# Performance work log

Measured on AMD Instinct MI355X. Metric: run time of the kernel, lower is better.

Reference implementation:

```python
import jax, jax.numpy as jnp
import numpy as np
from jax import lax

B, S, D, H = 8, 1024, 512, 8
K = 25  # moving-average kernel
EPS = 1e-6


def setup_inputs() -> dict:
    key = jax.random.key(0)
    ks = jax.random.split(key, 8)

    def dense_w(k, din, dout):
        return (jax.random.normal(k, (din, dout), jnp.float32) / np.sqrt(din).astype(np.float32))

    return {
        "x": jax.random.normal(ks[0], (B, S, D), jnp.float32),
        "wq": dense_w(ks[1], D, D), "bq": jnp.zeros((D,), jnp.float32),
        "wk": dense_w(ks[2], D, D), "bk": jnp.zeros((D,), jnp.float32),
        "wv": dense_w(ks[3], D, D), "bv": jnp.zeros((D,), jnp.float32),
        "wo": dense_w(ks[4], D, D), "bo": jnp.zeros((D,), jnp.float32),
        "w1": dense_w(ks[5], D, 4 * D), "b1": jnp.zeros((4 * D,), jnp.float32),
        "w2": dense_w(ks[6], 4 * D, D), "b2": jnp.zeros((D,), jnp.float32),
        "g1": jnp.ones((D,), jnp.float32), "be1": jnp.zeros((D,), jnp.float32),
        "g2": jnp.ones((D,), jnp.float32), "be2": jnp.zeros((D,), jnp.float32),
        "g3": jnp.ones((D,), jnp.float32), "be3": jnp.zeros((D,), jnp.float32),
        "num_heads": H,
    }


def _moving_avg(x):
    # TF AveragePooling1D(pool=K, stride=1, padding='same'): divisor excludes padding.
    s = lax.reduce_window(x, 0.0, lax.add, (1, K, 1), (1, 1, 1), 'SAME')
    cnt = lax.reduce_window(jnp.ones((1, x.shape[1], 1), x.dtype), 0.0, lax.add,
                            (1, K, 1), (1, 1, 1), 'SAME')
    return s / cnt


def _layernorm(x, g, b):
    m = jnp.mean(x, -1, keepdims=True)
    v = jnp.var(x, -1, keepdims=True)
    return (x - m) * jax.lax.rsqrt(v + EPS) * g + b


def _auto_correlation(x, wq, bq, wk, bk, wv, bv, wo, bo, num_heads):
    b, s, d = x.shape
    dp = d // num_heads
    def split_heads(t):
        return t.reshape(b, s, num_heads, dp).transpose(0, 2, 1, 3)  # [B,H,S,dp]
    q = split_heads(x @ wq + bq)
    k = split_heads(x @ wk + bk)
    v = split_heads(x @ wv + bv)
    # Faithful to source: rfft over innermost (depth) axis, fft_length = 2*S.
    qf = jnp.fft.rfft(q, n=2 * s, axis=-1)
    kf = jnp.fft.rfft(k, n=2 * s, axis=-1)
    corr = jnp.fft.irfft(qf * jnp.conj(kf), n=2 * s, axis=-1)[..., :s]  # [B,H,S,S]
    scale = 1.0 / np.sqrt(dp).astype(np.float32)
    attn = jax.nn.softmax(scale * corr, axis=-1)
    out = jnp.einsum('bhst,bhtd->bhsd', attn, v)
    out = out.transpose(0, 2, 1, 3).reshape(b, s, d)
    return out @ wo + bo


def reference(x, wq, bq, wk, bk, wv, bv, wo, bo, w1, b1, w2, b2,
              g1, be1, g2, be2, g3, be3, num_heads):
    trend_init = _moving_avg(x)
    seasonal_init = x - trend_init
    attn_out = _auto_correlation(seasonal_init, wq, bq, wk, bk, wv, bv, wo, bo, num_heads)
    out1 = _layernorm(attn_out + seasonal_init, g1, be1)
    ffn = jax.nn.relu(out1 @ w1 + b1) @ w2 + b2
    seasonal_out = _layernorm(out1 + ffn, g2, be2) + seasonal_init
    trend2 = _moving_avg(seasonal_out)
    seasonal_final = seasonal_out - trend2
    x_out = seasonal_final + (trend2 + trend_init)
    return _layernorm(x_out, g3, be3)
```

## Files before the change

kernel.cpp:

```cpp
#include <hip/hip_runtime.h>
#include <cstdint>


typedef float f32x4 __attribute__((ext_vector_type(4)));
typedef __bf16 bf16x8 __attribute__((ext_vector_type(8)));
typedef _Float16 h2t __attribute__((ext_vector_type(2)));
typedef unsigned short u16;
typedef unsigned int u32;
typedef u32 u32x4 __attribute__((ext_vector_type(4)));

__device__ __forceinline__ u16 f2bf(float f) {
  unsigned int u = __float_as_uint(f);
  u = (u + 0x7FFFu + ((u >> 16) & 1u)) >> 16;
  return (u16)u;
}

__device__ __forceinline__ float bf2f(u16 b) { return __uint_as_float((u32)b << 16); }

__device__ __forceinline__ u16 f2h(float f) {
  _Float16 hv = (_Float16)f;
  u16 b;
  __builtin_memcpy(&b, &hv, 2);
  return b;
}

__device__ __forceinline__ float dot2h(u32 qp, u32 kp_, float c) {
#if __has_builtin(__builtin_amdgcn_fdot2)
  return __builtin_amdgcn_fdot2(__builtin_bit_cast(h2t, qp),
                                __builtin_bit_cast(h2t, kp_), c, false);
#else
  h2t q = __builtin_bit_cast(h2t, qp), k = __builtin_bit_cast(h2t, kp_);
  c = fmaf((float)q.x, (float)k.x, c);
  return fmaf((float)q.y, (float)k.y, c);
#endif
}

__device__ __forceinline__ void gload_lds16(const void* g, void* l) {
  __builtin_amdgcn_global_load_lds((__attribute__((address_space(1))) void*)g,
                                   (__attribute__((address_space(3))) void*)l,
                                   16, 0, 0);
}

__global__ __launch_bounds__(256) void movavg_kernel(
    const float* __restrict__ x, u16* __restrict__ seas_bf,
    u16* __restrict__ a64, float* __restrict__ srow) {
  int blk = blockIdx.x;
  int sc = blk & 127, b = blk >> 7;
  int d = threadIdx.x * 2;
  const float* xb = x + (size_t)b * 1024 * 512 + d;
  int s0 = sc * 8;
  int lo = max(s0 - 12, 0), hi = min(s0 + 12, 1023);
  float sx = 0.f, sy = 0.f;
  for (int j = lo; j <= hi; ++j) {
    float2 v = *(const float2*)&xb[(size_t)j * 512];
    sx += v.x;
    sy += v.y;
  }
  float ax = 0.f, ay = 0.f;
#pragma unroll
  for (int s = s0; s < s0 + 8; ++s) {
    int l2 = max(s - 12, 0), h2 = min(s + 12, 1023);
    float invc = 1.f / (float)(h2 - l2 + 1);
    float2 xv = *(const float2*)&xb[(size_t)s * 512];
    float sex = xv.x - sx * invc;
    float sey = xv.y - sy * invc;
    size_t idx = (size_t)(b * 1024 + s) * 512 + d;
    u32 pk = (u32)f2bf(sex) | ((u32)f2bf(sey) << 16);
    *(u32*)&seas_bf[idx] = pk;
    if (s < 64) *(u32*)&a64[(size_t)(b * 64 + s) * 512 + d] = pk;
    ax += sex;
    ay += sey;
    if (s - 12 >= 0) {
      float2 v = *(const float2*)&xb[(size_t)(s - 12) * 512];
      sx -= v.x;
      sy -= v.y;
    }
    if (s + 13 <= 1023) {
      float2 v = *(const float2*)&xb[(size_t)(s + 13) * 512];
      sx += v.x;
      sy += v.y;
    }
  }
  atomicAdd(&srow[b * 512 + d], ax);
  atomicAdd(&srow[b * 512 + d + 1], ay);
}

__global__ __launch_bounds__(256) void weights_prep_kernel(
    const float* __restrict__ wq, const float* __restrict__ wk,
    const float* __restrict__ wv, const float* __restrict__ wo,
    const float* __restrict__ w1, const float* __restrict__ w2,
    const float* __restrict__ bq, const float* __restrict__ bk,
    u16* __restrict__ wqkt, u16* __restrict__ wvt, u16* __restrict__ wot,
    u16* __restrict__ w1t, u16* __restrict__ w2t, float* __restrict__ qkbias) {
  __shared__ float tile[32][33];
  int i = blockIdx.x;
  int tx = threadIdx.x, ty = threadIdx.y;
  if (i >= 3072) {
    int idx = (i - 3072) * 256 + ty * 32 + tx;
    qkbias[idx] = idx < 512 ? bq[idx] : bk[idx - 512];
    return;
  }
  const float* src;
  u16* dst;
  int R, C, bx, by;
  if (i < 1024) {
    int w = i >> 8, l = i & 255;
    src = (w == 0 ? wq : w == 1 ? wk : w == 2 ? wv : wo);
    dst = (w == 0 ? wqkt : w == 1 ? wqkt + 512 * 512 : w == 2 ? wvt : wot);
    R = 512; C = 512; bx = l & 15; by = l >> 4;
  } else if (i < 2048) {
    int l = i - 1024;
    src = w1; dst = w1t; R = 512; C = 2048; bx = l & 15; by = l >> 4;
  } else {
    int l = i - 2048;
    src = w2; dst = w2t; R = 2048; C = 512; bx = l & 63; by = l >> 6;
  }
  int r0 = bx * 32, c0 = by * 32;
#pragma unroll
  for (int k = 0; k < 4; ++k)
    tile[ty + 8 * k][tx] = src[(size_t)(r0 + ty + 8 * k) * C + c0 + tx];
  __syncthreads();
#pragma unroll
  for (int k = 0; k < 4; ++k)
    dst[(size_t)(c0 + ty + 8 * k) * R + r0 + tx] = f2bf(tile[tx][ty + 8 * k]);
}

__global__ __launch_bounds__(256) void vsum_kernel(
    const float* __restrict__ srow, const float* __restrict__ wv,
    const float* __restrict__ bv, float* __restrict__ vsum) {
  int blk = blockIdx.x;
  int b = blk >> 1;
  int n = (blk & 1) * 256 + threadIdx.x;
  float acc = 0.f;
  for (int k = 0; k < 512; ++k) acc += srow[b * 512 + k] * wv[(size_t)k * 512 + n];
  vsum[b * 512 + n] = acc + 1024.f * bv[n];
}

template <int RELU, int OMODE, int KSPLIT>
__global__ __launch_bounds__(512, 1) void gemm8p_kernel(
    const u16* __restrict__ A, const u16* __restrict__ Bt,
    const float* __restrict__ bias, void* __restrict__ Cv, void* __restrict__ Cv2,
    int M, int N, int K) {
  __shared__ u16 As[3][2][256 * 32];
  __shared__ u16 Bs[3][2][128 * 32];
  const int tid = threadIdx.x;
  const int wid = tid >> 6, lane = tid & 63;
  const int wm = wid >> 2, wn = wid & 3;
  const int la = lane & 15, lg = lane >> 4;
  int nwg = gridDim.x * gridDim.y;
  int lin = blockIdx.y * gridDim.x + blockIdx.x;
  int swz = (lin & 7) * (nwg >> 3) + (lin >> 3);
  int bx = swz / gridDim.y, by = swz % gridDim.y;
  const int row0 = bx * 256, col0 = by * 128;
  const int z = (KSPLIT > 1) ? (int)blockIdx.z : 0;
  const int kbeg = z * (K / KSPLIT);
  const int nt = (K / KSPLIT) / 64;
  f32x4 acc[8][2] = {};

  auto stageh = [&](int buf, int h, int k0) {
    int kh = k0 + h * 32;
    {
      int p = tid, r = p >> 2, cg = (p & 3) ^ ((r >> 1) & 3);
      gload_lds16(A + (size_t)(row0 + r) * K + kh + cg * 8,
                  ((char*)&As[buf][h][0]) + p * 16);
    }
    {
      int p = tid + 512, r = p >> 2, cg = (p & 3) ^ ((r >> 1) & 3);
      gload_lds16(A + (size_t)(row0 + r) * K + kh + cg * 8,
                  ((char*)&As[buf][h][0]) + p * 16);
    }
    {
      int p = tid, r = p >> 2, cg = (p & 3) ^ ((r >> 1) & 3);
      gload_lds16(Bt + (size_t)(col0 + r) * K + kh + cg * 8,
                  ((char*)&Bs[buf][h][0]) + p * 16);
    }
  };

  stageh(0, 0, kbeg);
  stageh(0, 1, kbeg);
  stageh(1, 0, kbeg + 64);
  stageh(1, 1, kbeg + 64);
  asm volatile("s_waitcnt vmcnt(6)" ::: "memory");
  __builtin_amdgcn_s_barrier();
  __builtin_amdgcn_sched_barrier(0);

  for (int t = 0; t < nt; ++t) {
    const int buf = t % 3;
    const int nbuf = (t + 2) % 3;
    const bool pre = (t + 2 < nt);
#pragma unroll
    for (int h = 0; h < 2; ++h) {
      bf16x8 af[8], bf[2];
#pragma unroll
      for (int mf = 0; mf < 8; ++mf) {
        int r = wm * 128 + mf * 16 + la;
        int cp = lg ^ ((r >> 1) & 3);
        af[mf] = *(const bf16x8*)&As[buf][h][r * 32 + cp * 8];
      }
#pragma unroll
      for (int nf = 0; nf < 2; ++nf) {
        int r = wn * 32 + nf * 16 + la;
        int cp = lg ^ ((r >> 1) & 3);
        bf[nf] = *(const bf16x8*)&Bs[buf][h][r * 32 + cp * 8];
      }
      if (pre) stageh(nbuf, h, kbeg + (t + 2) * 64);
      __builtin_amdgcn_sched_barrier(0);
      __builtin_amdgcn_s_barrier();
      __builtin_amdgcn_s_setprio(1);
#pragma unroll
      for (int mf = 0; mf < 8; ++mf)
#pragma unroll
        for (int nf = 0; nf < 2; ++nf)
          acc[mf][nf] = __builtin_amdgcn_mfma_f32_16x16x32_bf16(af[mf], bf[nf], acc[mf][nf], 0, 0, 0);
      __builtin_amdgcn_s_setprio(0);
      __builtin_amdgcn_sched_barrier(0);
      if (h == 0) __builtin_amdgcn_s_barrier();
    }
    if (pre)
      asm volatile("s_waitcnt vmcnt(6)" ::: "memory");
    else if (t + 1 < nt)
      asm volatile("s_waitcnt vmcnt(0)" ::: "memory");
    __builtin_amdgcn_s_barrier();
    __builtin_amdgcn_sched_barrier(0);
  }

  void* Cout = (z == 0) ? Cv : Cv2;
#pragma unroll
  for (int mf = 0; mf < 8; ++mf) {
    int r = row0 + wm * 128 + mf * 16 + lg * 4;
#pragma unroll
    for (int nf = 0; nf < 2; ++nf) {
      int cc = col0 + wn * 32 + nf * 16 + la;
      float bvv = (z == 0) ? bias[cc] : 0.f;
#pragma unroll
      for (int j = 0; j < 4; ++j) {
        float v = acc[mf][nf][j] + bvv;
        if (RELU) v = fmaxf(v, 0.f);
        if constexpr (OMODE == 1)
          ((u16*)Cout)[(size_t)(r + j) * N + cc] = f2bf(v);
        else
          ((u16*)Cout)[(size_t)(r + j) * N + cc] = f2h(v);
      }
    }
  }
}

__global__ __launch_bounds__(256, 6) void gemm_v_kernel(
    const u16* __restrict__ A, const u16* __restrict__ Bt,
    const float* __restrict__ bias, u16* __restrict__ Cv, int M, int N, int K) {
  constexpr int BK = 32;
  __shared__ u16 As[2][128 * BK];
  __shared__ u16 Bs[2][64 * BK];
  const int tid = threadIdx.x;
  const int wid = tid >> 6, lane = tid & 63;
  const int wm = wid >> 1, wn = wid & 1;
  const int la = lane & 15, lg = lane >> 4;
  const int row0 = blockIdx.x * 128, col0 = blockIdx.y * 64;
  const int ksteps = K / BK;
  f32x4 acc[4][2] = {};

  auto stage = [&](int buf, int k0) {
    {
      int p = tid, r = p >> 2, cg = (p & 3) ^ ((r >> 1) & 3);
      gload_lds16(A + (size_t)(row0 + r) * K + k0 + cg * 8, ((char*)As[buf]) + p * 16);
    }
    {
      int p = tid + 256, r = p >> 2, cg = (p & 3) ^ ((r >> 1) & 3);
      gload_lds16(A + (size_t)(row0 + r) * K + k0 + cg * 8, ((char*)As[buf]) + p * 16);
    }
    {
      int p = tid, r = p >> 2, cg = (p & 3) ^ ((r >> 1) & 3);
      gload_lds16(Bt + (size_t)(col0 + r) * K + k0 + cg * 8, ((char*)Bs[buf]) + p * 16);
    }
  };

  stage(0, 0);
  __syncthreads();
  for (int t = 0; t < ksteps; ++t) {
    const int cur = t & 1;
    if (t + 1 < ksteps) stage(cur ^ 1, (t + 1) * BK);
    bf16x8 af[4], bfr[2];
#pragma unroll
    for (int m = 0; m < 4; ++m) {
      int r = wm * 64 + m * 16 + la;
      int cp = lg ^ ((r >> 1) & 3);
      af[m] = *(const bf16x8*)(((const char*)As[cur]) + r * 64 + cp * 16);
    }
#pragma unroll
    for (int n = 0; n < 2; ++n) {
      int r = wn * 32 + n * 16 + la;
      int cp = lg ^ ((r >> 1) & 3);
      bfr[n] = *(const bf16x8*)(((const char*)Bs[cur]) + r * 64 + cp * 16);
    }
#pragma unroll
    for (int m = 0; m < 4; ++m)
#pragma unroll
      for (int n = 0; n < 2; ++n)
        acc[m][n] = __builtin_amdgcn_mfma_f32_16x16x32_bf16(af[m], bfr[n], acc[m][n], 0, 0, 0);
    __syncthreads();
  }

#pragma unroll
  for (int m = 0; m < 4; ++m) {
    int r = row0 + wm * 64 + m * 16 + lg * 4;
#pragma unroll
    for (int n = 0; n < 2; ++n) {
      int cc = col0 + wn * 32 + n * 16 + la;
      float bvv = bias[cc];
#pragma unroll
      for (int j = 0; j < 4; ++j) {
        float v = acc[m][n][j] + bvv;
        int rr = r + j;
        int bb = rr >> 6, tt = rr & 63, hh = cc >> 6, dd = cc & 63;
        Cv[(((size_t)bb * 8 + hh) * 64 + dd) * 64 + tt] = f2bf(v);
      }
    }
  }
}

__global__ __launch_bounds__(256) void attn_mfma_kernel(
    const u16* __restrict__ qk, const u16* __restrict__ v64t,
    const float* __restrict__ vsum, u16* __restrict__ attn_bf) {
  __shared__ u32 qE[32][64];
  __shared__ u32 qO[32][64];
  __shared__ u32 kp[32][32];
  __shared__ u16 coef[32][64];
  __shared__ u16 vtt[64][64];
  __shared__ float zc[32];
  __shared__ float Vs[64];
  int bid = blockIdx.x;
  int scnk = bid & 31, h = (bid >> 5) & 7, b = bid >> 8;
  int tid = threadIdx.x, wid = tid >> 6, lane = tid & 63;
  int bh = b * 8 + h;

  {
    int p = tid, r = p >> 3, cc = p & 7;
    gload_lds16(v64t + ((size_t)bh * 4096 + r * 64 + ((cc ^ (r & 7)) * 8)),
                ((char*)vtt) + p * 16);
    p = tid + 256; r = p >> 3; cc = p & 7;
    gload_lds16(v64t + ((size_t)bh * 4096 + r * 64 + ((cc ^ (r & 7)) * 8)),
                ((char*)vtt) + p * 16);
  }
  *(f32x4*)&qE[tid >> 3][32 + ((tid & 7) << 2)] = f32x4{};
  {
    int s = tid >> 3, c = tid & 7;
    size_t grow = ((size_t)(b * 1024 + scnk * 32 + s)) * 1024 + h * 64;
    *(f32x4*)&qE[s][c * 4] = *(const f32x4*)&qk[grow + c * 8];
    *(f32x4*)&kp[s][c * 4] = *(const f32x4*)&qk[grow + 512 + c * 8];
  }
  if (tid < 64) Vs[tid] = vsum[b * 512 + h * 64 + tid];
  __syncthreads();
  for (int j2 = tid; j2 < 1024; j2 += 256) {
    int s = j2 >> 5, j = j2 & 31;
    u32 a = qE[s][j], b2 = qE[s][j + 1];
    qO[s][j] = (a >> 16) | (b2 << 16);
    qO[s][j + 32] = 0;
  }
  __syncthreads();
  for (int i = 0; i < 8; ++i) {
    int s = wid * 8 + i;
    u32x4 kk4[8];
#pragma unroll
    for (int u = 0; u < 8; ++u) kk4[u] = *(const u32x4*)&kp[s][u * 4];
    int t = lane, sel = t & 1;
    const u32* qptr = (sel ? qO[s] : qE[s]) + (t >> 1);
    float c = 0.f;
#pragma unroll
    for (int u = 0; u < 8; ++u) {
#pragma unroll
      for (int v = 0; v < 4; ++v) c = dot2h(qptr[u * 4 + v], kk4[u][v], c);
    }
    float sc = c * 0.125f;
    float mx = fmaxf(sc, 0.f);
#pragma unroll
    for (int off = 32; off >= 1; off >>= 1) mx = fmaxf(mx, __shfl_xor(mx, off));
    float w = __expf(sc - mx), wz = __expf(-mx);
    float sw = w;
#pragma unroll
    for (int off = 32; off >= 1; off >>= 1) sw += __shfl_xor(sw, off);
    float inv = 1.f / (sw + 960.f * wz);
    *(u16*)(((char*)&coef[s][0]) + ((2 * t) ^ ((s & 7) << 4))) = f2bf((w - wz) * inv);
    if (lane == 0) zc[s] = wz * inv;
  }
  __syncthreads();
  {
    int sm = wid >> 1, nh = wid & 1;
    int la = lane & 15, lg = lane >> 4;
    int r = sm * 16 + la;
    int n0 = nh * 32 + la, n1 = nh * 32 + 16 + la;
    f32x4 acc0 = {}, acc1 = {};
#pragma unroll
    for (int ks = 0; ks < 2; ++ks) {
      int lr = ks * 4 + lg;
      bf16x8 af = *(const bf16x8*)(((const char*)coef) + r * 128 + ((lr ^ (r & 7)) << 4));
      bf16x8 bf0 = *(const bf16x8*)(((const char*)vtt) + n0 * 128 + ((lr ^ (n0 & 7)) << 4));
      bf16x8 bf1 = *(const bf16x8*)(((const char*)vtt) + n1 * 128 + ((lr ^ (n1 & 7)) << 4));
      acc0 = __builtin_amdgcn_mfma_f32_16x16x32_bf16(af, bf0, acc0, 0, 0, 0);
      acc1 = __builtin_amdgcn_mfma_f32_16x16x32_bf16(af, bf1, acc1, 0, 0, 0);
    }
    int srl0 = sm * 16 + lg * 4;
    int srow0 = b * 1024 + scnk * 32 + srl0;
    float vs0 = Vs[nh * 32 + la], vs1 = Vs[nh * 32 + 16 + la];
#pragma unroll
    for (int j = 0; j < 4; ++j) {
      float zcv = zc[srl0 + j];
      size_t rb = (size_t)(srow0 + j) * 512 + h * 64;
      attn_bf[rb + nh * 32 + la] = f2bf(acc0[j] + zcv * vs0);
      attn_bf[rb + nh * 32 + 16 + la] = f2bf(acc1[j] + zcv * vs1);
    }
  }
}

__device__ __forceinline__ void block_reduce_2(float& a, float& b, float* sbuf) {
  int tid = threadIdx.x, wid = tid >> 6, lane = tid & 63;
#pragma unroll
  for (int off = 32; off >= 1; off >>= 1) {
    a += __shfl_xor(a, off);
    b += __shfl_xor(b, off);
  }
  if (lane == 0) {
    sbuf[wid] = a;
    sbuf[4 + wid] = b;
  }
  __syncthreads();
  a = sbuf[0] + sbuf[1] + sbuf[2] + sbuf[3];
  b = sbuf[4] + sbuf[5] + sbuf[6] + sbuf[7];
  __syncthreads();
}

__global__ __launch_bounds__(256) void ln_res_kernel(
    const u16* __restrict__ xa, const u16* __restrict__ xb,
    u16* __restrict__ res_out,
    const float* __restrict__ g, const float* __restrict__ be) {
  __shared__ float sbuf[8];
  int row = blockIdx.x, tid = threadIdx.x;
  int d = tid * 2;
  size_t base = (size_t)row * 512 + d;
  u32 pa = *(const u32*)&xa[base];
  u32 pb = *(const u32*)&xb[base];
  u32 pr = *(const u32*)&res_out[base];
  float v0 = bf2f((u16)pa) + bf2f((u16)pb) + bf2f((u16)pr);
  float v1 = bf2f((u16)(pa >> 16)) + bf2f((u16)(pb >> 16)) + bf2f((u16)(pr >> 16));
  float s = v0 + v1, q = v0 * v0 + v1 * v1;
  block_reduce_2(s, q, sbuf);
  float mean = s * (1.f / 512.f);
  float var = q * (1.f / 512.f) - mean * mean;
  float rs = rsqrtf(var + 1e-6f);
  float2 gg = *(const float2*)&g[d];
  float2 bb = *(const float2*)&be[d];
  float o0 = (v0 - mean) * rs * gg.x + bb.x;
  float o1 = (v1 - mean) * rs * gg.y + bb.y;
  *(u32*)&res_out[base] = (u32)f2bf(o0) | ((u32)f2bf(o1) << 16);
}

__global__ __launch_bounds__(256) void final_kernel(
    const u16* __restrict__ out1, const u16* __restrict__ fa,
    const u16* __restrict__ fb, const float* __restrict__ x,
    const float* __restrict__ g2, const float* __restrict__ be2,
    const float* __restrict__ g3, const float* __restrict__ be3,
    float* __restrict__ out) {
  __shared__ float sbuf[8];
  int row = blockIdx.x, tid = threadIdx.x;
  int d = tid * 2;
  size_t base = (size_t)row * 512 + d;
  u32 po = *(const u32*)&out1[base];
  u32 pa = *(const u32*)&fa[base];
  u32 pb = *(const u32*)&fb[base];
  float t0 = bf2f((u16)po) + bf2f((u16)pa) + bf2f((u16)pb);
  float t1 = bf2f((u16)(po >> 16)) + bf2f((u16)(pa >> 16)) + bf2f((u16)(pb >> 16));
  float s = t0 + t1, q = t0 * t0 + t1 * t1;
  block_reduce_2(s, q, sbuf);
  float mean = s * (1.f / 512.f);
  float var = q * (1.f / 512.f) - mean * mean;
  float rs = rsqrtf(var + 1e-6f);
  float2 g2v = *(const float2*)&g2[d];
  float2 b2v = *(const float2*)&be2[d];
  float2 xv = *(const float2*)&x[base];
  float y0 = (t0 - mean) * rs * g2v.x + b2v.x + xv.x;
  float y1 = (t1 - mean) * rs * g2v.y + b2v.y + xv.y;
  s = y0 + y1;
  q = y0 * y0 + y1 * y1;
  block_reduce_2(s, q, sbuf);
  mean = s * (1.f / 512.f);
  var = q * (1.f / 512.f) - mean * mean;
  rs = rsqrtf(var + 1e-6f);
  float2 g3v = *(const float2*)&g3[d];
  float2 b3v = *(const float2*)&be3[d];
  float2 o = make_float2((y0 - mean) * rs * g3v.x + b3v.x,
                         (y1 - mean) * rs * g3v.y + b3v.y);
  *(float2*)&out[base] = o;
}

extern "C" void kernel_launch(void* const* d_in, const int* in_sizes, int n_in,
                              void* d_out, int out_size, void* d_ws, size_t ws_size,
                              hipStream_t stream) {
  const float* x = (const float*)d_in[0];
  const float* wq = (const float*)d_in[1];
  const float* bq = (const float*)d_in[2];
  const float* wk = (const float*)d_in[3];
  const float* bk = (const float*)d_in[4];
  const float* wv = (const float*)d_in[5];
  const float* bv = (const float*)d_in[6];
  const float* wo = (const float*)d_in[7];
  const float* bo = (const float*)d_in[8];
  const float* w1 = (const float*)d_in[9];
  const float* b1 = (const float*)d_in[10];
  const float* w2 = (const float*)d_in[11];
  const float* b2 = (const float*)d_in[12];
  const float* g1 = (const float*)d_in[13];
  const float* be1 = (const float*)d_in[14];
  const float* g2 = (const float*)d_in[15];
  const float* be2 = (const float*)d_in[16];
  const float* g3 = (const float*)d_in[17];
  const float* be3 = (const float*)d_in[18];
  float* out = (float*)d_out;

  const size_t MS = 8192ull * 512ull;
  float* srow = (float*)d_ws;
  float* vsumb = srow + 4096;
  float* qkbias = vsumb + 4096;
  u16* qk_f16 = (u16*)(qkbias + 1024);
  u16* hidden = qk_f16 + 8192ull * 1024;
  u16* seas_bf = hidden + 8192ull * 2048;
  u16* attn_bf = seas_bf + MS;
  u16* wo0 = attn_bf + MS;
  u16* wo1 = wo0 + MS;
  u16* v64t = wo1 + MS;
  u16* a64_bf = v64t + 512 * 512;
  u16* wqkt = a64_bf + 512 * 512;
  u16* wvt = wqkt + 1024 * 512;
  u16* wot = wvt + 512 * 512;
  u16* w1t = wot + 512 * 512;
  u16* w2t = w1t + 2048ull * 512;
  u16* ff0 = qk_f16;
  u16* ff1 = ff0 + MS;

  hipMemsetAsync(srow, 0, 4096 * sizeof(float), stream);
  weights_prep_kernel<<<3076, dim3(32, 8), 0, stream>>>(
      wq, wk, wv, wo, w1, w2, bq, bk, wqkt, wvt, wot, w1t, w2t, qkbias);

  movavg_kernel<<<1024, 256, 0, stream>>>(x, seas_bf, a64_bf, srow);
  vsum_kernel<<<16, 256, 0, stream>>>(srow, wv, bv, vsumb);

  gemm8p_kernel<0, 2, 1><<<dim3(32, 8), 512, 0, stream>>>(
      seas_bf, wqkt, qkbias, qk_f16, nullptr, 8192, 1024, 512);
  gemm_v_kernel<<<dim3(4, 8), 256, 0, stream>>>(a64_bf, wvt, bv, v64t, 512, 512, 512);

  attn_mfma_kernel<<<2048, 256, 0, stream>>>(qk_f16, v64t, vsumb, attn_bf);

  gemm8p_kernel<0, 1, 2><<<dim3(32, 4, 2), 512, 0, stream>>>(
      attn_bf, wot, bo, wo0, wo1, 8192, 512, 512);
  ln_res_kernel<<<8192, 256, 0, stream>>>(wo0, wo1, seas_bf, g1, be1);

  gemm8p_kernel<1, 1, 1><<<dim3(32, 16), 512, 0, stream>>>(
      seas_bf, w1t, b1, hidden, nullptr, 8192, 2048, 512);
  gemm8p_kernel<0, 1, 2><<<dim3(32, 4, 2), 512, 0, stream>>>(
      hidden, w2t, b2, ff0, ff1, 8192, 512, 2048);

  final_kernel<<<8192, 256, 0, stream>>>(seas_bf, ff0, ff1, x, g2, be2, g3, be3, out);
}
```

Before: 212.3 us.

## Fuse QK projection GEMM with auto-correlation attention in one kernel

Replaces the separate Q/K projection GEMM and the attention kernel with one kernel. Each block computes the Q and K columns for one head over 256 rows, keeps the fp16 results in LDS, then runs the correlation, softmax and V product from that LDS tile. This removes the global round trip of the 8192x1024 qk_f16 intermediate and one kernel launch. In exchange it uses about 156KB of LDS, so only one block runs per CU, and the grid is just 256 blocks. The attention phase also runs serially over eight chunks inside each block.

```diff
diff --git a/kernel.cpp b/kernel.cpp
--- a/kernel.cpp
+++ b/kernel.cpp
@@ -236,12 +236,203 @@
       for (int j = 0; j < 4; ++j) {
         float v = acc[mf][nf][j] + bvv;
         if (RELU) v = fmaxf(v, 0.f);
-        if constexpr (OMODE == 1)
-          ((u16*)Cout)[(size_t)(r + j) * N + cc] = f2bf(v);
-        else
-          ((u16*)Cout)[(size_t)(r + j) * N + cc] = f2h(v);
-      }
-    }
+        ((u16*)Cout)[(size_t)(r + j) * N + cc] = f2bf(v);
+      }
+    }
+  }
+}
+
+__global__ __launch_bounds__(512, 1) void qkattn_kernel(
+    const u16* __restrict__ A, const u16* __restrict__ Wqk,
+    const float* __restrict__ qkb, const u16* __restrict__ v64t,
+    const float* __restrict__ vsum, u16* __restrict__ attn_bf) {
+  __shared__ __align__(16) char pool[156160];
+  u16* vtt = (u16*)(pool + 147456);
+  float* Vs = (float*)(pool + 155648);
+  float* zc = (float*)(pool + 155904);
+  u16* tile = (u16*)pool;
+  u32* qE = (u32*)(pool + 65536);
+  u32* qO = (u32*)(pool + 73728);
+  u32* kp = (u32*)(pool + 81920);
+  u16* coef = (u16*)(pool + 86016);
+
+  const int tid = threadIdx.x;
+  const int wid = tid >> 6, lane = tid & 63;
+  const int wm = wid >> 2, wn = wid & 3;
+  const int la = lane & 15, lg = lane >> 4;
+  const int K = 512;
+  int nwg = gridDim.x * gridDim.y;
+  int lin = blockIdx.y * gridDim.x + blockIdx.x;
+  int swz = (lin & 7) * (nwg >> 3) + (lin >> 3);
+  int bx = swz / gridDim.y, h = swz % gridDim.y;
+  const int row0 = bx * 256;
+  const int b = row0 >> 10;
+  const int bh = b * 8 + h;
+  f32x4 acc[8][2] = {};
+
+  {
+    int p = tid, r = p >> 3, cc = p & 7;
+    gload_lds16(v64t + ((size_t)bh * 4096 + r * 64 + ((cc ^ (r & 7)) * 8)),
+                ((char*)vtt) + p * 16);
+  }
+
+  auto stageh = [&](int buf, int hh, int k0) {
+    int kh = k0 + hh * 32;
+    char* abase = pool + (buf * 2 + hh) * 16384;
+    char* bbase = pool + 98304 + (buf * 2 + hh) * 8192;
+    {
+      int p = tid, r = p >> 2, cg = (p & 3) ^ ((r >> 1) & 3);
+      gload_lds16(A + (size_t)(row0 + r) * K + kh + cg * 8, abase + p * 16);
+    }
+    {
+      int p = tid + 512, r = p >> 2, cg = (p & 3) ^ ((r >> 1) & 3);
+      gload_lds16(A + (size_t)(row0 + r) * K + kh + cg * 8, abase + p * 16);
+    }
+    {
+      int p = tid, r = p >> 2, cg = (p & 3) ^ ((r >> 1) & 3);
+      int gr = (r < 64) ? h * 64 + r : 448 + h * 64 + r;
+      gload_lds16(Wqk + (size_t)gr * K + kh + cg * 8, bbase + p * 16);
+    }
+  };
+
+  stageh(0, 0, 0);
+  stageh(0, 1, 0);
+  stageh(1, 0, 64);
+  stageh(1, 1, 64);
+  asm volatile("s_waitcnt vmcnt(6)" ::: "memory");
+  __builtin_amdgcn_s_barrier();
+  __builtin_amdgcn_sched_barrier(0);
+
+  const int nt = 8;
+  for (int t = 0; t < nt; ++t) {
+    const int buf = t % 3, nbuf = (t + 2) % 3;
+    const bool pre = (t + 2 < nt);
+#pragma unroll
+    for (int hh = 0; hh < 2; ++hh) {
+      const char* ab = pool + (buf * 2 + hh) * 16384;
+      const char* bb = pool + 98304 + (buf * 2 + hh) * 8192;
+      bf16x8 af[8], bfv[2];
+#pragma unroll
+      for (int mf = 0; mf < 8; ++mf) {
+        int r = wm * 128 + mf * 16 + la;
+        int cp = lg ^ ((r >> 1) & 3);
+        af[mf] = *(const bf16x8*)(ab + r * 64 + cp * 16);
+      }
+#pragma unroll
+      for (int nf = 0; nf < 2; ++nf) {
+        int r = wn * 32 + nf * 16 + la;
+        int cp = lg ^ ((r >> 1) & 3);
+        bfv[nf] = *(const bf16x8*)(bb + r * 64 + cp * 16);
+      }
+      if (pre) stageh(nbuf, hh, (t + 2) * 64);
+      __builtin_amdgcn_sched_barrier(0);
+      __builtin_amdgcn_s_barrier();
+      __builtin_amdgcn_s_setprio(1);
+#pragma unroll
+      for (int mf = 0; mf < 8; ++mf)
+#pragma unroll
+        for (int nf = 0; nf < 2; ++nf)
+          acc[mf][nf] = __builtin_amdgcn_mfma_f32_16x16x32_bf16(af[mf], bfv[nf], acc[mf][nf], 0, 0, 0);
+      __builtin_amdgcn_s_setprio(0);
+      __builtin_amdgcn_sched_barrier(0);
+      if (hh == 0) __builtin_amdgcn_s_barrier();
+    }
+    if (pre)
+      asm volatile("s_waitcnt vmcnt(6)" ::: "memory");
+    else if (t + 1 < nt)
+      asm volatile("s_waitcnt vmcnt(0)" ::: "memory");
+    __builtin_amdgcn_s_barrier();
+    __builtin_amdgcn_sched_barrier(0);
+  }
+  if (tid < 64) Vs[tid] = vsum[b * 512 + h * 64 + tid];
+#pragma unroll
+  for (int mf = 0; mf < 8; ++mf) {
+    int r = wm * 128 + mf * 16 + lg * 4;
+#pragma unroll
+    for (int nf = 0; nf < 2; ++nf) {
+      int cc = wn * 32 + nf * 16 + la;
+      float bvv = qkb[(cc < 64) ? h * 64 + cc : 448 + h * 64 + cc];
+#pragma unroll
+      for (int j = 0; j < 4; ++j) {
+        int rr = r + j;
+        u32 byte = ((u32)(rr * 128 + cc) * 2) ^ ((u32)(rr & 7) << 4);
+        *(u16*)(((char*)tile) + byte) = f2h(acc[mf][nf][j] + bvv);
+      }
+    }
+  }
+  __builtin_amdgcn_s_barrier();
+
+  for (int c = 0; c < 8; ++c) {
+    int cr0 = c * 32;
+    for (int idx = tid; idx < 2048; idx += 512) {
+      int s = idx >> 6, j = idx & 63;
+      u32 v = 0;
+      if (j < 32) {
+        int rr = cr0 + s;
+        u32 byte = ((u32)(rr * 128 + 2 * j) * 2) ^ ((u32)(rr & 7) << 4);
+        v = *(const u32*)(((const char*)tile) + byte);
+      }
+      qE[s * 64 + j] = v;
+    }
+    for (int idx = tid; idx < 1024; idx += 512) {
+      int s = idx >> 5, m = idx & 31;
+      int rr = cr0 + s;
+      u32 byte = ((u32)(rr * 128 + 64 + 2 * m) * 2) ^ ((u32)(rr & 7) << 4);
+      kp[s * 32 + m] = *(const u32*)(((const char*)tile) + byte);
+    }
+    __builtin_amdgcn_s_barrier();
+    for (int idx = tid; idx < 1024; idx += 512) {
+      int s = idx >> 5, j = idx & 31;
+      u32 a = qE[s * 64 + j], b2 = qE[s * 64 + j + 1];
+      qO[s * 64 + j] = (a >> 16) | (b2 << 16);
+      qO[s * 64 + j + 32] = 0;
+    }
+    __builtin_amdgcn_s_barrier();
+    for (int i = 0; i < 4; ++i) {
+      int s = wid * 4 + i;
+      u32x4 kk4[8];
+#pragma unroll
+      for (int u = 0; u < 8; ++u) kk4[u] = *(const u32x4*)&kp[s * 32 + u * 4];
+      int t2 = lane, sel = t2 & 1;
+      const u32* qptr = (sel ? qO : qE) + s * 64 + (t2 >> 1);
+      float cv = 0.f;
+#pragma unroll
+      for (int u = 0; u < 8; ++u)
+#pragma unroll
+        for (int v = 0; v < 4; ++v) cv = dot2h(qptr[u * 4 + v], kk4[u][v], cv);
+      float sc = cv * 0.125f;
+      float mx = fmaxf(sc, 0.f);
+#pragma unroll
+      for (int off = 32; off >= 1; off >>= 1) mx = fmaxf(mx, __shfl_xor(mx, off));
+      float w = __expf(sc - mx), wz = __expf(-mx);
+      float sw = w;
+#pragma unroll
+      for (int off = 32; off >= 1; off >>= 1) sw += __shfl_xor(sw, off);
+      float inv = 1.f / (sw + 960.f * wz);
+      *(u16*)(((char*)coef) + ((s * 128 + 2 * t2) ^ ((s & 7) << 4))) = f2bf((w - wz) * inv);
+      if (lane == 0) zc[s] = wz * inv;
+    }
+    __builtin_amdgcn_s_barrier();
+    {
+      int sm = wid >> 2, nh = wid & 3;
+      int r = sm * 16 + la;
+      int n0 = nh * 16 + la;
+      f32x4 a0 = {};
+#pragma unroll
+      for (int ks = 0; ks < 2; ++ks) {
+        int lr = ks * 4 + lg;
+        bf16x8 af = *(const bf16x8*)(((const char*)coef) + r * 128 + ((lr ^ (r & 7)) << 4));
+        bf16x8 b0 = *(const bf16x8*)(((const char*)vtt) + n0 * 128 + ((lr ^ (n0 & 7)) << 4));
+        a0 = __builtin_amdgcn_mfma_f32_16x16x32_bf16(af, b0, a0, 0, 0, 0);
+      }
+      int srl0 = sm * 16 + lg * 4;
+      int srow0 = row0 + cr0 + srl0;
+      float vs0 = Vs[n0];
+#pragma unroll
+      for (int j = 0; j < 4; ++j)
+        attn_bf[(size_t)(srow0 + j) * 512 + h * 64 + n0] = f2bf(a0[j] + zc[srl0 + j] * vs0);
+    }
+    __builtin_amdgcn_s_barrier();
   }
 }
 
@@ -314,99 +505,6 @@
         int bb = rr >> 6, tt = rr & 63, hh = cc >> 6, dd = cc & 63;
         Cv[(((size_t)bb * 8 + hh) * 64 + dd) * 64 + tt] = f2bf(v);
       }
-    }
-  }
-}
-
-__global__ __launch_bounds__(256) void attn_mfma_kernel(
-    const u16* __restrict__ qk, const u16* __restrict__ v64t,
-    const float* __restrict__ vsum, u16* __restrict__ attn_bf) {
-  __shared__ u32 qE[32][64];
-  __shared__ u32 qO[32][64];
-  __shared__ u32 kp[32][32];
-  __shared__ u16 coef[32][64];
-  __shared__ u16 vtt[64][64];
-  __shared__ float zc[32];
-  __shared__ float Vs[64];
-  int bid = blockIdx.x;
-  int scnk = bid & 31, h = (bid >> 5) & 7, b = bid >> 8;
-  int tid = threadIdx.x, wid = tid >> 6, lane = tid & 63;
-  int bh = b * 8 + h;
-
-  {
-    int p = tid, r = p >> 3, cc = p & 7;
-    gload_lds16(v64t + ((size_t)bh * 4096 + r * 64 + ((cc ^ (r & 7)) * 8)),
-                ((char*)vtt) + p * 16);
-    p = tid + 256; r = p >> 3; cc = p & 7;
-    gload_lds16(v64t + ((size_t)bh * 4096 + r * 64 + ((cc ^ (r & 7)) * 8)),
-                ((char*)vtt) + p * 16);
-  }
-  *(f32x4*)&qE[tid >> 3][32 + ((tid & 7) << 2)] = f32x4{};
-  {
-    int s = tid >> 3, c = tid & 7;
-    size_t grow = ((size_t)(b * 1024 + scnk * 32 + s)) * 1024 + h * 64;
-    *(f32x4*)&qE[s][c * 4] = *(const f32x4*)&qk[grow + c * 8];
-    *(f32x4*)&kp[s][c * 4] = *(const f32x4*)&qk[grow + 512 + c * 8];
-  }
-  if (tid < 64) Vs[tid] = vsum[b * 512 + h * 64 + tid];
-  __syncthreads();
-  for (int j2 = tid; j2 < 1024; j2 += 256) {
-    int s = j2 >> 5, j = j2 & 31;
-    u32 a = qE[s][j], b2 = qE[s][j + 1];
-    qO[s][j] = (a >> 16) | (b2 << 16);
-    qO[s][j + 32] = 0;
-  }
-  __syncthreads();
-  for (int i = 0; i < 8; ++i) {
-    int s = wid * 8 + i;
-    u32x4 kk4[8];
-#pragma unroll
-    for (int u = 0; u < 8; ++u) kk4[u] = *(const u32x4*)&kp[s][u * 4];
-    int t = lane, sel = t & 1;
-    const u32* qptr = (sel ? qO[s] : qE[s]) + (t >> 1);
-    float c = 0.f;
-#pragma unroll
-    for (int u = 0; u < 8; ++u) {
-#pragma unroll
-      for (int v = 0; v < 4; ++v) c = dot2h(qptr[u * 4 + v], kk4[u][v], c);
-    }
-    float sc = c * 0.125f;
-    float mx = fmaxf(sc, 0.f);
-#pragma unroll
-    for (int off = 32; off >= 1; off >>= 1) mx = fmaxf(mx, __shfl_xor(mx, off));
-    float w = __expf(sc - mx), wz = __expf(-mx);
-    float sw = w;
-#pragma unroll
-    for (int off = 32; off >= 1; off >>= 1) sw += __shfl_xor(sw, off);
-    float inv = 1.f / (sw + 960.f * wz);
-    *(u16*)(((char*)&coef[s][0]) + ((2 * t) ^ ((s & 7) << 4))) = f2bf((w - wz) * inv);
-    if (lane == 0) zc[s] = wz * inv;
-  }
-  __syncthreads();
-  {
-    int sm = wid >> 1, nh = wid & 1;
-    int la = lane & 15, lg = lane >> 4;
-    int r = sm * 16 + la;
-    int n0 = nh * 32 + la, n1 = nh * 32 + 16 + la;
-    f32x4 acc0 = {}, acc1 = {};
-#pragma unroll
-    for (int ks = 0; ks < 2; ++ks) {
-      int lr = ks * 4 + lg;
-      bf16x8 af = *(const bf16x8*)(((const char*)coef) + r * 128 + ((lr ^ (r & 7)) << 4));
-      bf16x8 bf0 = *(const bf16x8*)(((const char*)vtt) + n0 * 128 + ((lr ^ (n0 & 7)) << 4));
-      bf16x8 bf1 = *(const bf16x8*)(((const char*)vtt) + n1 * 128 + ((lr ^ (n1 & 7)) << 4));
-      acc0 = __builtin_amdgcn_mfma_f32_16x16x32_bf16(af, bf0, acc0, 0, 0, 0);
-      acc1 = __builtin_amdgcn_mfma_f32_16x16x32_bf16(af, bf1, acc1, 0, 0, 0);
-    }
-    int srl0 = sm * 16 + lg * 4;
-    int srow0 = b * 1024 + scnk * 32 + srl0;
-    float vs0 = Vs[nh * 32 + la], vs1 = Vs[nh * 32 + 16 + la];
-#pragma unroll
-    for (int j = 0; j < 4; ++j) {
-      float zcv = zc[srl0 + j];
-      size_t rb = (size_t)(srow0 + j) * 512 + h * 64;
-      attn_bf[rb + nh * 32 + la] = f2bf(acc0[j] + zcv * vs0);
-      attn_bf[rb + nh * 32 + 16 + la] = f2bf(acc1[j] + zcv * vs1);
     }
   }
 }
@@ -519,8 +617,8 @@
   float* srow = (float*)d_ws;
   float* vsumb = srow + 4096;
   float* qkbias = vsumb + 4096;
-  u16* qk_f16 = (u16*)(qkbias + 1024);
-  u16* hidden = qk_f16 + 8192ull * 1024;
+  u16* ffbuf = (u16*)(qkbias + 1024);
+  u16* hidden = ffbuf + 2 * MS;
   u16* seas_bf = hidden + 8192ull * 2048;
   u16* attn_bf = seas_bf + MS;
   u16* wo0 = attn_bf + MS;
@@ -532,7 +630,7 @@
   u16* wot = wvt + 512 * 512;
   u16* w1t = wot + 512 * 512;
   u16* w2t = w1t + 2048ull * 512;
-  u16* ff0 = qk_f16;
+  u16* ff0 = ffbuf;
   u16* ff1 = ff0 + MS;
 
   hipMemsetAsync(srow, 0, 4096 * sizeof(float), stream);
@@ -542,11 +640,9 @@
   movavg_kernel<<<1024, 256, 0, stream>>>(x, seas_bf, a64_bf, srow);
   vsum_kernel<<<16, 256, 0, stream>>>(srow, wv, bv, vsumb);
 
-  gemm8p_kernel<0, 2, 1><<<dim3(32, 8), 512, 0, stream>>>(
-      seas_bf, wqkt, qkbias, qk_f16, nullptr, 8192, 1024, 512);
   gemm_v_kernel<<<dim3(4, 8), 256, 0, stream>>>(a64_bf, wvt, bv, v64t, 512, 512, 512);
-
-  attn_mfma_kernel<<<2048, 256, 0, stream>>>(qk_f16, v64t, vsumb, attn_bf);
+  qkattn_kernel<<<dim3(32, 8), 512, 0, stream>>>(
+      seas_bf, wqkt, qkbias, v64t, vsumb, attn_bf);
 
   gemm8p_kernel<0, 1, 2><<<dim3(32, 4, 2), 512, 0, stream>>>(
       attn_bf, wot, bo, wo0, wo1, 8192, 512, 512);
```

New measurement: 212.5 us. No clear change (+0.1%).

## Merge moving-average into prep kernel, halve attention row chunk, unroll vsum

Applied to the files above, without the earlier changes.

Folds the moving-average/seasonal kernel into the weight-prep launch as extra blocks, which removes one kernel launch and lets the two independent jobs run concurrently. The attention kernel now handles 16 query rows per block instead of 32 and launches twice as many blocks, for more parallelism and less shared memory per block, at the cost of reloading the V tile more often. The vsum reduction is split across eight independent FMA accumulators to expose more instruction-level parallelism.

```diff
diff --git a/kernel.cpp b/kernel.cpp
--- a/kernel.cpp
+++ b/kernel.cpp
@@ -41,62 +41,63 @@
                                    16, 0, 0);
 }
 
-__global__ __launch_bounds__(256) void movavg_kernel(
-    const float* __restrict__ x, u16* __restrict__ seas_bf,
-    u16* __restrict__ a64, float* __restrict__ srow) {
-  int blk = blockIdx.x;
-  int sc = blk & 127, b = blk >> 7;
-  int d = threadIdx.x * 2;
-  const float* xb = x + (size_t)b * 1024 * 512 + d;
-  int s0 = sc * 8;
-  int lo = max(s0 - 12, 0), hi = min(s0 + 12, 1023);
-  float sx = 0.f, sy = 0.f;
-  for (int j = lo; j <= hi; ++j) {
-    float2 v = *(const float2*)&xb[(size_t)j * 512];
-    sx += v.x;
-    sy += v.y;
-  }
-  float ax = 0.f, ay = 0.f;
-#pragma unroll
-  for (int s = s0; s < s0 + 8; ++s) {
-    int l2 = max(s - 12, 0), h2 = min(s + 12, 1023);
-    float invc = 1.f / (float)(h2 - l2 + 1);
-    float2 xv = *(const float2*)&xb[(size_t)s * 512];
-    float sex = xv.x - sx * invc;
-    float sey = xv.y - sy * invc;
-    size_t idx = (size_t)(b * 1024 + s) * 512 + d;
-    u32 pk = (u32)f2bf(sex) | ((u32)f2bf(sey) << 16);
-    *(u32*)&seas_bf[idx] = pk;
-    if (s < 64) *(u32*)&a64[(size_t)(b * 64 + s) * 512 + d] = pk;
-    ax += sex;
-    ay += sey;
-    if (s - 12 >= 0) {
-      float2 v = *(const float2*)&xb[(size_t)(s - 12) * 512];
-      sx -= v.x;
-      sy -= v.y;
-    }
-    if (s + 13 <= 1023) {
-      float2 v = *(const float2*)&xb[(size_t)(s + 13) * 512];
-      sx += v.x;
-      sy += v.y;
-    }
-  }
-  atomicAdd(&srow[b * 512 + d], ax);
-  atomicAdd(&srow[b * 512 + d + 1], ay);
-}
-
-__global__ __launch_bounds__(256) void weights_prep_kernel(
+__global__ __launch_bounds__(256) void prep_kernel(
     const float* __restrict__ wq, const float* __restrict__ wk,
     const float* __restrict__ wv, const float* __restrict__ wo,
     const float* __restrict__ w1, const float* __restrict__ w2,
     const float* __restrict__ bq, const float* __restrict__ bk,
     u16* __restrict__ wqkt, u16* __restrict__ wvt, u16* __restrict__ wot,
-    u16* __restrict__ w1t, u16* __restrict__ w2t, float* __restrict__ qkbias) {
+    u16* __restrict__ w1t, u16* __restrict__ w2t, float* __restrict__ qkbias,
+    const float* __restrict__ x, u16* __restrict__ seas_bf,
+    u16* __restrict__ a64, float* __restrict__ srow) {
   __shared__ float tile[32][33];
   int i = blockIdx.x;
-  int tx = threadIdx.x, ty = threadIdx.y;
+  int tid = threadIdx.x;
+  int tx = tid & 31, ty = tid >> 5;
+  if (i >= 3076) {
+    int blk = i - 3076;
+    int sc = blk & 127, b = blk >> 7;
+    int d = tid * 2;
+    const float* xb = x + (size_t)b * 1024 * 512 + d;
+    int s0 = sc * 8;
+    int lo = max(s0 - 12, 0), hi = min(s0 + 12, 1023);
+    float sx = 0.f, sy = 0.f;
+    for (int j = lo; j <= hi; ++j) {
+      float2 v = *(const float2*)&xb[(size_t)j * 512];
+      sx += v.x;
+      sy += v.y;
+    }
+    float ax = 0.f, ay = 0.f;
+#pragma unroll
+    for (int s = s0; s < s0 + 8; ++s) {
+      int l2 = max(s - 12, 0), h2 = min(s + 12, 1023);
+      float invc = 1.f / (float)(h2 - l2 + 1);
+      float2 xv = *(const float2*)&xb[(size_t)s * 512];
+      float sex = xv.x - sx * invc;
+      float sey = xv.y - sy * invc;
+      size_t idx = (size_t)(b * 1024 + s) * 512 + d;
+      u32 pk = (u32)f2bf(sex) | ((u32)f2bf(sey) << 16);
+      *(u32*)&seas_bf[idx] = pk;
+      if (s < 64) *(u32*)&a64[(size_t)(b * 64 + s) * 512 + d] = pk;
+      ax += sex;
+      ay += sey;
+      if (s - 12 >= 0) {
+        float2 v = *(const float2*)&xb[(size_t)(s - 12) * 512];
+        sx -= v.x;
+        sy -= v.y;
+      }
+      if (s + 13 <= 1023) {
+        float2 v = *(const float2*)&xb[(size_t)(s + 13) * 512];
+        sx += v.x;
+        sy += v.y;
+      }
+    }
+    atomicAdd(&srow[b * 512 + d], ax);
+    atomicAdd(&srow[b * 512 + d + 1], ay);
+    return;
+  }
   if (i >= 3072) {
-    int idx = (i - 3072) * 256 + ty * 32 + tx;
+    int idx = (i - 3072) * 256 + tid;
     qkbias[idx] = idx < 512 ? bq[idx] : bk[idx - 512];
     return;
   }
@@ -131,9 +132,20 @@
   int blk = blockIdx.x;
   int b = blk >> 1;
   int n = (blk & 1) * 256 + threadIdx.x;
-  float acc = 0.f;
-  for (int k = 0; k < 512; ++k) acc += srow[b * 512 + k] * wv[(size_t)k * 512 + n];
-  vsum[b * 512 + n] = acc + 1024.f * bv[n];
+  float a0 = 0.f, a1 = 0.f, a2 = 0.f, a3 = 0.f;
+  float a4 = 0.f, a5 = 0.f, a6 = 0.f, a7 = 0.f;
+  const float* sr = srow + b * 512;
+  for (int k = 0; k < 512; k += 8) {
+    a0 = fmaf(sr[k + 0], wv[(size_t)(k + 0) * 512 + n], a0);
+    a1 = fmaf(sr[k + 1], wv[(size_t)(k + 1) * 512 + n], a1);
+    a2 = fmaf(sr[k + 2], wv[(size_t)(k + 2) * 512 + n], a2);
+    a3 = fmaf(sr[k + 3], wv[(size_t)(k + 3) * 512 + n], a3);
+    a4 = fmaf(sr[k + 4], wv[(size_t)(k + 4) * 512 + n], a4);
+    a5 = fmaf(sr[k + 5], wv[(size_t)(k + 5) * 512 + n], a5);
+    a6 = fmaf(sr[k + 6], wv[(size_t)(k + 6) * 512 + n], a6);
+    a7 = fmaf(sr[k + 7], wv[(size_t)(k + 7) * 512 + n], a7);
+  }
+  vsum[b * 512 + n] = ((a0 + a1) + (a2 + a3)) + ((a4 + a5) + (a6 + a7)) + 1024.f * bv[n];
 }
 
 template <int RELU, int OMODE, int KSPLIT>
@@ -321,17 +333,18 @@
 __global__ __launch_bounds__(256) void attn_mfma_kernel(
     const u16* __restrict__ qk, const u16* __restrict__ v64t,
     const float* __restrict__ vsum, u16* __restrict__ attn_bf) {
-  __shared__ u32 qE[32][64];
-  __shared__ u32 qO[32][64];
-  __shared__ u32 kp[32][32];
-  __shared__ u16 coef[32][64];
+  __shared__ u32 qE[16][64];
+  __shared__ u32 qO[16][64];
+  __shared__ u32 kp[16][32];
+  __shared__ u16 coef[16][64];
   __shared__ u16 vtt[64][64];
-  __shared__ float zc[32];
+  __shared__ float zc[16];
   __shared__ float Vs[64];
   int bid = blockIdx.x;
-  int scnk = bid & 31, h = (bid >> 5) & 7, b = bid >> 8;
+  int scnk = bid & 63, h = (bid >> 6) & 7, b = bid >> 9;
   int tid = threadIdx.x, wid = tid >> 6, lane = tid & 63;
   int bh = b * 8 + h;
+  int row0 = b * 1024 + scnk * 16;
 
   {
     int p = tid, r = p >> 3, cc = p & 7;
@@ -341,24 +354,33 @@
     gload_lds16(v64t + ((size_t)bh * 4096 + r * 64 + ((cc ^ (r & 7)) * 8)),
                 ((char*)vtt) + p * 16);
   }
-  *(f32x4*)&qE[tid >> 3][32 + ((tid & 7) << 2)] = f32x4{};
+  for (int idx = tid; idx < 512; idx += 256) {
+    int s = idx >> 5, j = (idx & 31) + 32;
+    qE[s][j] = 0;
+  }
   {
-    int s = tid >> 3, c = tid & 7;
-    size_t grow = ((size_t)(b * 1024 + scnk * 32 + s)) * 1024 + h * 64;
-    *(f32x4*)&qE[s][c * 4] = *(const f32x4*)&qk[grow + c * 8];
-    *(f32x4*)&kp[s][c * 4] = *(const f32x4*)&qk[grow + 512 + c * 8];
+    if (tid < 128) {
+      int s = tid >> 3, c = tid & 7;
+      size_t grow = ((size_t)(row0 + s)) * 1024 + h * 64;
+      *(f32x4*)&qE[s][c * 4] = *(const f32x4*)&qk[grow + c * 8];
+    } else {
+      int t2 = tid - 128;
+      int s = t2 >> 3, c = t2 & 7;
+      size_t grow = ((size_t)(row0 + s)) * 1024 + 512 + h * 64;
+      *(f32x4*)&kp[s][c * 4] = *(const f32x4*)&qk[grow + c * 8];
+    }
   }
   if (tid < 64) Vs[tid] = vsum[b * 512 + h * 64 + tid];
   __syncthreads();
-  for (int j2 = tid; j2 < 1024; j2 += 256) {
-    int s = j2 >> 5, j = j2 & 31;
+  for (int idx = tid; idx < 512; idx += 256) {
+    int s = idx >> 5, j = idx & 31;
     u32 a = qE[s][j], b2 = qE[s][j + 1];
     qO[s][j] = (a >> 16) | (b2 << 16);
     qO[s][j + 32] = 0;
   }
   __syncthreads();
-  for (int i = 0; i < 8; ++i) {
-    int s = wid * 8 + i;
+  for (int i = 0; i < 4; ++i) {
+    int s = wid * 4 + i;
     u32x4 kk4[8];
 #pragma unroll
     for (int u = 0; u < 8; ++u) kk4[u] = *(const u32x4*)&kp[s][u * 4];
@@ -384,29 +406,23 @@
   }
   __syncthreads();
   {
-    int sm = wid >> 1, nh = wid & 1;
     int la = lane & 15, lg = lane >> 4;
-    int r = sm * 16 + la;
-    int n0 = nh * 32 + la, n1 = nh * 32 + 16 + la;
-    f32x4 acc0 = {}, acc1 = {};
+    int r = la;
+    int n0 = wid * 16 + la;
+    f32x4 a0 = {};
 #pragma unroll
     for (int ks = 0; ks < 2; ++ks) {
       int lr = ks * 4 + lg;
       bf16x8 af = *(const bf16x8*)(((const char*)coef) + r * 128 + ((lr ^ (r & 7)) << 4));
-      bf16x8 bf0 = *(const bf16x8*)(((const char*)vtt) + n0 * 128 + ((lr ^ (n0 & 7)) << 4));
-      bf16x8 bf1 = *(const bf16x8*)(((const char*)vtt) + n1 * 128 + ((lr ^ (n1 & 7)) << 4));
-      acc0 = __builtin_amdgcn_mfma_f32_16x16x32_bf16(af, bf0, acc0, 0, 0, 0);
-      acc1 = __builtin_amdgcn_mfma_f32_16x16x32_bf16(af, bf1, acc1, 0, 0, 0);
-    }
-    int srl0 = sm * 16 + lg * 4;
-    int srow0 = b * 1024 + scnk * 32 + srl0;
-    float vs0 = Vs[nh * 32 + la], vs1 = Vs[nh * 32 + 16 + la];
+      bf16x8 b0 = *(const bf16x8*)(((const char*)vtt) + n0 * 128 + ((lr ^ (n0 & 7)) << 4));
+      a0 = __builtin_amdgcn_mfma_f32_16x16x32_bf16(af, b0, a0, 0, 0, 0);
+    }
+    int srl0 = lg * 4;
+    float vs0 = Vs[wid * 16 + la];
 #pragma unroll
     for (int j = 0; j < 4; ++j) {
-      float zcv = zc[srl0 + j];
-      size_t rb = (size_t)(srow0 + j) * 512 + h * 64;
-      attn_bf[rb + nh * 32 + la] = f2bf(acc0[j] + zcv * vs0);
-      attn_bf[rb + nh * 32 + 16 + la] = f2bf(acc1[j] + zcv * vs1);
+      size_t rb = (size_t)(row0 + srl0 + j) * 512 + h * 64;
+      attn_bf[rb + wid * 16 + la] = f2bf(a0[j] + zc[srl0 + j] * vs0);
     }
   }
 }
@@ -536,17 +552,16 @@
   u16* ff1 = ff0 + MS;
 
   hipMemsetAsync(srow, 0, 4096 * sizeof(float), stream);
-  weights_prep_kernel<<<3076, dim3(32, 8), 0, stream>>>(
-      wq, wk, wv, wo, w1, w2, bq, bk, wqkt, wvt, wot, w1t, w2t, qkbias);
-
-  movavg_kernel<<<1024, 256, 0, stream>>>(x, seas_bf, a64_bf, srow);
+  prep_kernel<<<4100, 256, 0, stream>>>(
+      wq, wk, wv, wo, w1, w2, bq, bk, wqkt, wvt, wot, w1t, w2t, qkbias,
+      x, seas_bf, a64_bf, srow);
   vsum_kernel<<<16, 256, 0, stream>>>(srow, wv, bv, vsumb);
 
   gemm8p_kernel<0, 2, 1><<<dim3(32, 8), 512, 0, stream>>>(
       seas_bf, wqkt, qkbias, qk_f16, nullptr, 8192, 1024, 512);
   gemm_v_kernel<<<dim3(4, 8), 256, 0, stream>>>(a64_bf, wvt, bv, v64t, 512, 512, 512);
 
-  attn_mfma_kernel<<<2048, 256, 0, stream>>>(qk_f16, v64t, vsumb, attn_bf);
+  attn_mfma_kernel<<<4096, 256, 0, stream>>>(qk_f16, v64t, vsumb, attn_bf);
 
   gemm8p_kernel<0, 1, 2><<<dim3(32, 4, 2), 512, 0, stream>>>(
       attn_bf, wot, bo, wo0, wo1, 8192, 512, 512);
```

Result: faster. 203.1 us (-4.4%).
